# Optimization experiments

Hardware: AMD Instinct MI355X
Metric: run time of the kernel (lower is better)

## Reference

```python
import jax, jax.numpy as jnp
import numpy as np

BS, SL, NC = 512, 1024, 64


def setup_inputs() -> dict:
    key = jax.random.key(0)
    k1, k2, k3, k4 = jax.random.split(key, 4)
    inputs = jax.random.normal(k1, (BS, SL, NC), dtype=jnp.float32)
    # valid-suffix padding masks: True = padded position (as in the torch module)
    lengths = jax.random.randint(k2, (BS,), SL // 2, SL + 1)
    masks = jnp.arange(SL)[None, :] >= lengths[:, None]  # bool [BS, SL]
    tag_indices = jax.random.randint(k3, (BS, SL), 0, NC).astype(jnp.int64)
    transitions = jax.random.normal(k4, (NC, NC), dtype=jnp.float32) * 0.01
    return {"inputs": inputs, "masks": masks, "tag_indices": tag_indices,
            "transitions": transitions}


def _crf_loss(inputs, masks, tag_indices, transitions):
    bs, sl, nc = inputs.shape
    # unary score: emission at gold tag per step, padded steps zeroed
    unary = jnp.take_along_axis(inputs, tag_indices[..., None], axis=2)[..., 0]
    unary = jnp.where(masks, 0.0, unary).sum(axis=1)  # [bs]
    # binary score: transition between consecutive gold tags
    binary = transitions[tag_indices[:, :-1], tag_indices[:, 1:]]  # [bs, sl-1]
    binary = jnp.where(masks[:, 1:], 0.0, binary).sum(axis=1)  # [bs]
    # log partition via forward algorithm (lax.scan over time)
    def step(alphas, xs):
        x_t, m_t = xs  # [bs, nc], [bs]
        scores = alphas[:, :, None] + transitions[None, :, :]  # [bs, nc(from), nc(to)]
        new_alphas = x_t + jax.nn.logsumexp(scores, axis=1)
        alphas = jnp.where(m_t[:, None], alphas, new_alphas)
        return alphas, None

    xs = (jnp.swapaxes(inputs[:, 1:, :], 0, 1), jnp.swapaxes(masks[:, 1:], 0, 1))
    alphas, _ = jax.lax.scan(step, inputs[:, 0, :], xs)
    log_norm = jax.nn.logsumexp(alphas, axis=1)  # [bs]
    log_likelihood = unary + binary - log_norm
    loss = jnp.sum(-log_likelihood) / bs  # batch_average=True
    return loss


def reference(inputs, masks, tag_indices, transitions):
    loss = _crf_loss(inputs, masks, tag_indices, transitions)
    return (loss, transitions)
```

## Files before the change

### kernel.cpp

```cpp
#include <hip/hip_runtime.h>

#define BS 512
#define SL 1024
#define NC 64

__global__ __launch_bounds__(256) void crf_init_out(const float* __restrict__ trans,
                                                    float* __restrict__ out) {
    int idx = blockIdx.x * 256 + threadIdx.x;
    if (idx == 0) out[0] = 0.0f;
    if (idx < NC * NC) out[1 + idx] = trans[idx];
}

__global__ __launch_bounds__(64) void crf_fwd(const float* __restrict__ inputs,
                                              const int* __restrict__ masks,
                                              const int* __restrict__ tags,
                                              const float* __restrict__ trans,
                                              float* __restrict__ out) {
    const int b = blockIdx.x;
    const int lane = threadIdx.x;

    __shared__ float Tlds[NC * NC];
    __shared__ float plds[NC];
    __shared__ float red[NC];
    __shared__ int   taglds[SL];
    __shared__ int   lenlds;

    const float* __restrict__ inrow = inputs + (size_t)b * SL * NC;

    float E[NC];
#pragma unroll
    for (int i = 0; i < NC; ++i) {
        float tv = trans[i * NC + lane];
        Tlds[i * NC + lane] = tv;
        E[i] = __expf(tv);
    }

    int cnt = 0;
#pragma unroll
    for (int k = 0; k < SL / NC; ++k) {
        int idx = k * NC + lane;
        taglds[idx] = tags[(size_t)b * SL + idx];
        cnt += (masks[(size_t)b * SL + idx] == 0) ? 1 : 0;
    }
    red[lane] = (float)cnt;
    __syncthreads();
    if (lane == 0) {
        int s = 0;
        for (int i = 0; i < NC; ++i) s += (int)red[i];
        lenlds = s;
    }
    __syncthreads();
    const int len = lenlds;

    float x = inrow[lane];
    float alpha = x;
    int tagprev = taglds[0];
    float u = (lane == tagprev) ? x : 0.0f;
    float bacc = 0.0f;

    float xcur = inrow[NC + lane];

    for (int t = 1; t < len; ++t) {
        int tn = t + 1; if (tn > SL - 1) tn = SL - 1;
        float xnext = inrow[tn * NC + lane];

        float a0 = __int_as_float(__builtin_amdgcn_readfirstlane(__float_as_int(alpha)));
        float p = __expf(alpha - a0);
        plds[lane] = p;
        __syncthreads();

        float s0 = 0.f, s1 = 0.f, s2 = 0.f, s3 = 0.f;
#pragma unroll
        for (int j = 0; j < NC / 4; ++j) {
            float4 pv = ((const float4*)plds)[j];
            s0 = fmaf(pv.x, E[4 * j + 0], s0);
            s1 = fmaf(pv.y, E[4 * j + 1], s1);
            s2 = fmaf(pv.z, E[4 * j + 2], s2);
            s3 = fmaf(pv.w, E[4 * j + 3], s3);
        }
        float s = (s0 + s1) + (s2 + s3);

        int tg = taglds[t];
        bacc += Tlds[tagprev * NC + tg];
        u += (lane == tg) ? xcur : 0.0f;

        alpha = xcur + a0 + __logf(s);
        tagprev = tg;
        xcur = xnext;
        __syncthreads();
    }

    float a0 = __int_as_float(__builtin_amdgcn_readfirstlane(__float_as_int(alpha)));
    plds[lane] = __expf(alpha - a0);
    red[lane] = u;
    __syncthreads();
    float s0 = 0.f, s1 = 0.f, s2 = 0.f, s3 = 0.f;
#pragma unroll
    for (int j = 0; j < NC / 4; ++j) {
        float4 pv = ((const float4*)plds)[j];
        s0 += pv.x; s1 += pv.y; s2 += pv.z; s3 += pv.w;
    }
    float log_norm = a0 + __logf((s0 + s1) + (s2 + s3));

    if (lane == 0) {
        float usum = 0.f;
        for (int i = 0; i < NC; ++i) usum += red[i];
        float ll = usum + bacc - log_norm;
        atomicAdd(out, -ll * (1.0f / BS));
    }
}

extern "C" void kernel_launch(void* const* d_in, const int* in_sizes, int n_in,
                              void* d_out, int out_size, void* d_ws, size_t ws_size,
                              hipStream_t stream) {
    const float* inputs = (const float*)d_in[0];
    const int*   masks  = (const int*)d_in[1];
    const int*   tags   = (const int*)d_in[2];
    const float* trans  = (const float*)d_in[3];
    float* out = (float*)d_out;

    crf_init_out<<<(1 + NC * NC + 255) / 256, 256, 0, stream>>>(trans, out);
    crf_fwd<<<BS, 64, 0, stream>>>(inputs, masks, tags, trans, out);
}
```

Measured before the change: 574.4 us.

## Replace LDS broadcast and barriers in CRF recurrence with DPP/permlane register exchange

The per-step broadcast of the 64 probabilities moves from shared memory plus two barriers per timestep to an in-register exchange built from permlane swaps and DPP moves. The transition exp matrix is pre-permuted per lane so each lane's received values line up with the right entries. The recurrence now runs in a scaled linear domain, renormalizing by lane 0's value and accumulating the log scale, with the emission exp prefetched two steps ahead. The mask length uses a ballot/popcount, and the final reductions use DPP wave sums. In exchange the code depends on DPP and permlane semantics being correct, and the linear-domain scaling may behave differently numerically from the log-domain form.

```diff
diff --git a/kernel.cpp b/kernel.cpp
--- a/kernel.cpp
+++ b/kernel.cpp
@@ -3,6 +3,48 @@
 #define BS 512
 #define SL 1024
 #define NC 64
+
+template <int CTRL>
+__device__ __forceinline__ float dppf(float x) {
+    return __int_as_float(__builtin_amdgcn_mov_dpp(__float_as_int(x), CTRL, 0xF, 0xF, true));
+}
+__device__ __forceinline__ float rflf(float x) {
+    return __int_as_float(__builtin_amdgcn_readfirstlane(__float_as_int(x)));
+}
+
+__device__ __forceinline__ void halfswap32(float x, float& r0, float& r1) {
+#if __has_builtin(__builtin_amdgcn_permlane32_swap)
+    auto r = __builtin_amdgcn_permlane32_swap(__float_as_int(x), __float_as_int(x), false, false);
+    r0 = __int_as_float(r[0]); r1 = __int_as_float(r[1]);
+#else
+    float w = __shfl_xor(x, 32, 64);
+    bool up = (threadIdx.x & 32) != 0;
+    r0 = up ? w : x;
+    r1 = up ? x : w;
+#endif
+}
+__device__ __forceinline__ void halfswap16(float x, float& r0, float& r1) {
+#if __has_builtin(__builtin_amdgcn_permlane16_swap)
+    auto r = __builtin_amdgcn_permlane16_swap(__float_as_int(x), __float_as_int(x), false, false);
+    r0 = __int_as_float(r[0]); r1 = __int_as_float(r[1]);
+#else
+    float w = __int_as_float(__builtin_amdgcn_ds_swizzle(__float_as_int(x), 0x401F));
+    bool up = (threadIdx.x & 16) != 0;
+    r0 = up ? w : x;
+    r1 = up ? x : w;
+#endif
+}
+
+__device__ __forceinline__ float wave_sum(float x) {
+    x += dppf<0xB1>(x);
+    x += dppf<0x4E>(x);
+    x += dppf<0x141>(x);
+    x += dppf<0x140>(x);
+    float a, c;
+    halfswap16(x, a, c); x = a + c;
+    halfswap32(x, a, c); x = a + c;
+    return x;
+}
 
 __global__ __launch_bounds__(256) void crf_init_out(const float* __restrict__ trans,
                                                     float* __restrict__ out) {
@@ -11,100 +53,135 @@
     if (idx < NC * NC) out[1 + idx] = trans[idx];
 }
 
-__global__ __launch_bounds__(64) void crf_fwd(const float* __restrict__ inputs,
-                                              const int* __restrict__ masks,
-                                              const int* __restrict__ tags,
-                                              const float* __restrict__ trans,
-                                              float* __restrict__ out) {
+__global__ __launch_bounds__(64, 1) void crf_fwd(const float* __restrict__ inputs,
+                                                 const int* __restrict__ masks,
+                                                 const int* __restrict__ tags,
+                                                 const float* __restrict__ trans,
+                                                 float* __restrict__ out) {
     const int b = blockIdx.x;
     const int lane = threadIdx.x;
 
     __shared__ float Tlds[NC * NC];
-    __shared__ float plds[NC];
-    __shared__ float red[NC];
     __shared__ int   taglds[SL];
-    __shared__ int   lenlds;
 
     const float* __restrict__ inrow = inputs + (size_t)b * SL * NC;
 
-    float E[NC];
-#pragma unroll
-    for (int i = 0; i < NC; ++i) {
-        float tv = trans[i * NC + lane];
-        Tlds[i * NC + lane] = tv;
-        E[i] = __expf(tv);
-    }
-
-    int cnt = 0;
+#pragma unroll
+    for (int i = 0; i < NC; ++i) Tlds[i * NC + lane] = trans[i * NC + lane];
+
+    int len = 0;
 #pragma unroll
     for (int k = 0; k < SL / NC; ++k) {
         int idx = k * NC + lane;
         taglds[idx] = tags[(size_t)b * SL + idx];
-        cnt += (masks[(size_t)b * SL + idx] == 0) ? 1 : 0;
-    }
-    red[lane] = (float)cnt;
+        unsigned long long bal = __ballot(masks[(size_t)b * SL + idx] == 0);
+        len += __popcll(bal);
+    }
     __syncthreads();
+
+    int B[4];
+    {
+        float pf = __int_as_float(lane);
+        float p0, p1, a0, a1, c0, c1;
+        halfswap32(pf, p0, p1);
+        halfswap16(p0, a0, a1);
+        halfswap16(p1, c0, c1);
+        B[0] = __builtin_amdgcn_readfirstlane(__float_as_int(a0));
+        B[1] = __builtin_amdgcn_readfirstlane(__float_as_int(a1));
+        B[2] = __builtin_amdgcn_readfirstlane(__float_as_int(c0));
+        B[3] = __builtin_amdgcn_readfirstlane(__float_as_int(c1));
+    }
+
+    float E[64];
+#pragma unroll
+    for (int f = 0; f < 4; ++f) {
+#pragma unroll
+        for (int m = 0; m < 16; ++m) {
+            int row = B[f] + ((lane ^ m) & 15);
+            E[f * 16 + m] = __expf(Tlds[row * NC + lane]);
+        }
+    }
+
+    float x0 = inrow[lane];
+    float base = rflf(x0);
+    float q = __expf(x0 - base);
+    int tagprev = taglds[0];
+    float u = (lane == tagprev) ? x0 : 0.0f;
+    float bacc = 0.0f;
+
+    int   tg_cur = taglds[1];
+    float x_cur = inrow[NC + lane];
+    float x_n1  = inrow[2 * NC + lane];
+    float ex_cur = __expf(x_cur);
+
+    for (int t = 1; t < len; ++t) {
+        int t2 = t + 2; if (t2 > SL - 1) t2 = SL - 1;
+        float x_n2 = inrow[(size_t)t2 * NC + lane];
+        int tn = t + 1; if (tn > SL - 1) tn = SL - 1;
+        int tg_next = taglds[tn];
+        float Tv = Tlds[tagprev * NC + tg_cur];
+        float ex_n1 = __expf(x_n1);
+
+        float m  = rflf(q);
+        float rm = __builtin_amdgcn_rcpf(m);
+        float ex_eff = ex_cur * rm;
+        base += __logf(m);
+
+        float v[64];
+        {
+            float u0, u1;
+            halfswap32(q, u0, u1);
+            halfswap16(u0, v[0],  v[16]);
+            halfswap16(u1, v[32], v[48]);
+#pragma unroll
+            for (int F = 0; F < 64; F += 16) {
+                v[F + 1]  = dppf<0xB1>(v[F + 0]);
+                v[F + 2]  = dppf<0x4E>(v[F + 0]);
+                v[F + 3]  = dppf<0x4E>(v[F + 1]);
+                v[F + 7]  = dppf<0x141>(v[F + 0]);
+                v[F + 6]  = dppf<0x141>(v[F + 1]);
+                v[F + 5]  = dppf<0x141>(v[F + 2]);
+                v[F + 4]  = dppf<0x141>(v[F + 3]);
+                v[F + 15] = dppf<0x140>(v[F + 0]);
+                v[F + 14] = dppf<0x140>(v[F + 1]);
+                v[F + 13] = dppf<0x140>(v[F + 2]);
+                v[F + 12] = dppf<0x140>(v[F + 3]);
+                v[F + 11] = dppf<0x140>(v[F + 4]);
+                v[F + 10] = dppf<0x140>(v[F + 5]);
+                v[F + 9]  = dppf<0x140>(v[F + 6]);
+                v[F + 8]  = dppf<0x140>(v[F + 7]);
+            }
+        }
+
+        float acc0 = 0.f, acc1 = 0.f, acc2 = 0.f, acc3 = 0.f;
+        float acc4 = 0.f, acc5 = 0.f, acc6 = 0.f, acc7 = 0.f;
+#pragma unroll
+        for (int j = 0; j < 64; j += 8) {
+            acc0 = fmaf(v[j + 0], E[j + 0], acc0);
+            acc1 = fmaf(v[j + 1], E[j + 1], acc1);
+            acc2 = fmaf(v[j + 2], E[j + 2], acc2);
+            acc3 = fmaf(v[j + 3], E[j + 3], acc3);
+            acc4 = fmaf(v[j + 4], E[j + 4], acc4);
+            acc5 = fmaf(v[j + 5], E[j + 5], acc5);
+            acc6 = fmaf(v[j + 6], E[j + 6], acc6);
+            acc7 = fmaf(v[j + 7], E[j + 7], acc7);
+        }
+        float s = ((acc0 + acc1) + (acc2 + acc3)) + ((acc4 + acc5) + (acc6 + acc7));
+
+        u += (lane == tg_cur) ? x_cur : 0.0f;
+        bacc += Tv;
+
+        q = s * ex_eff;
+
+        tagprev = tg_cur; tg_cur = tg_next;
+        x_cur = x_n1; x_n1 = x_n2; ex_cur = ex_n1;
+    }
+
+    float qsum = wave_sum(q);
+    float usum = wave_sum(u);
+    float log_norm = base + __logf(qsum);
+
     if (lane == 0) {
-        int s = 0;
-        for (int i = 0; i < NC; ++i) s += (int)red[i];
-        lenlds = s;
-    }
-    __syncthreads();
-    const int len = lenlds;
-
-    float x = inrow[lane];
-    float alpha = x;
-    int tagprev = taglds[0];
-    float u = (lane == tagprev) ? x : 0.0f;
-    float bacc = 0.0f;
-
-    float xcur = inrow[NC + lane];
-
-    for (int t = 1; t < len; ++t) {
-        int tn = t + 1; if (tn > SL - 1) tn = SL - 1;
-        float xnext = inrow[tn * NC + lane];
-
-        float a0 = __int_as_float(__builtin_amdgcn_readfirstlane(__float_as_int(alpha)));
-        float p = __expf(alpha - a0);
-        plds[lane] = p;
-        __syncthreads();
-
-        float s0 = 0.f, s1 = 0.f, s2 = 0.f, s3 = 0.f;
-#pragma unroll
-        for (int j = 0; j < NC / 4; ++j) {
-            float4 pv = ((const float4*)plds)[j];
-            s0 = fmaf(pv.x, E[4 * j + 0], s0);
-            s1 = fmaf(pv.y, E[4 * j + 1], s1);
-            s2 = fmaf(pv.z, E[4 * j + 2], s2);
-            s3 = fmaf(pv.w, E[4 * j + 3], s3);
-        }
-        float s = (s0 + s1) + (s2 + s3);
-
-        int tg = taglds[t];
-        bacc += Tlds[tagprev * NC + tg];
-        u += (lane == tg) ? xcur : 0.0f;
-
-        alpha = xcur + a0 + __logf(s);
-        tagprev = tg;
-        xcur = xnext;
-        __syncthreads();
-    }
-
-    float a0 = __int_as_float(__builtin_amdgcn_readfirstlane(__float_as_int(alpha)));
-    plds[lane] = __expf(alpha - a0);
-    red[lane] = u;
-    __syncthreads();
-    float s0 = 0.f, s1 = 0.f, s2 = 0.f, s3 = 0.f;
-#pragma unroll
-    for (int j = 0; j < NC / 4; ++j) {
-        float4 pv = ((const float4*)plds)[j];
-        s0 += pv.x; s1 += pv.y; s2 += pv.z; s3 += pv.w;
-    }
-    float log_norm = a0 + __logf((s0 + s1) + (s2 + s3));
-
-    if (lane == 0) {
-        float usum = 0.f;
-        for (int i = 0; i < NC; ++i) usum += red[i];
         float ll = usum + bacc - log_norm;
         atomicAdd(out, -ll * (1.0f / BS));
     }
```

New measurement: 592.3 us. 3.1% more time.
